# Performance work log

Hardware: AMD Instinct MI355X
Metric: run time of the kernel (lower is better)

Reference implementation:

```python
import jax, jax.numpy as jnp
import numpy as np

HIDDEN = 64
ALPHA = 0.2  # leaky relu negative slope
NEG_INF = -9e15


def setup_inputs() -> dict:
    key = jax.random.key(0)
    k1, k2, k3, k4, k5 = jax.random.split(key, 5)
    b, N, Fin, Fout = 8, 2048, 512, 256
    inp = jax.random.normal(k1, (b, N, Fin), dtype=jnp.float32)
    adj = jax.random.randint(k2, (b, N, N), 0, 2, dtype=jnp.int32)
    # xavier_uniform with gain=1.414 ~ uniform(-lim, lim)
    def xavier(k, shape):
        lim = 1.414 * np.sqrt(6.0 / (shape[0] + shape[1]))
        return jax.random.uniform(k, shape, jnp.float32, -lim, lim)
    weight = xavier(k3, (Fin, Fout))
    ht = xavier(k4, (Fout, HIDDEN))
    a = xavier(k5, (2 * HIDDEN, 1))
    return {"input": inp, "adj": adj, "weight": weight, "ht": ht, "a": a}


def reference(input, adj, weight, ht, a):
    # h: [b, N, Fout]
    h = jnp.matmul(input, weight)
    # trans_h: [b, N, HIDDEN]
    trans_h = jnp.einsum('bnc,ck->bnk', h, ht)
    # The original cat([th_i, th_j]) @ a decomposes as th_i@a1 + th_j@a2
    a1, a2 = a[:HIDDEN, 0], a[HIDDEN:, 0]
    f1 = trans_h @ a1  # [b, N] source (row) term
    f2 = trans_h @ a2  # [b, N] target (col) term
    e = f1[:, :, None] + f2[:, None, :]  # [b, N, N]
    e = jnp.where(e >= 0, e, ALPHA * e)  # leaky relu
    scores = jnp.where(adj > 0, e, NEG_INF)
    attention = jax.nn.softmax(scores, axis=2)
    # dropout is identity in eval mode (deterministic reference)
    h_prime = jnp.matmul(attention, h)  # [b, N, Fout]
    return jax.nn.elu(h_prime)  # concat=True
```

## Files before the change

kernel.cpp:

```cpp
#include <hip/hip_runtime.h>

typedef float f32x4 __attribute__((ext_vector_type(4)));
typedef short s16x8 __attribute__((ext_vector_type(8)));
typedef unsigned short u16x4 __attribute__((ext_vector_type(4)));

#define NB 8
#define NN 2048
#define FIN 512
#define FOUT 256

__device__ __forceinline__ unsigned short f2bf(float f) {
  unsigned u = __builtin_bit_cast(unsigned, f);
  u += 0x7fffu + ((u >> 16) & 1u);
  return (unsigned short)(u >> 16);
}

__global__ void prep_vecs_k(const float* __restrict__ W, const float* __restrict__ HT,
                            const float* __restrict__ A, float* __restrict__ v1,
                            float* __restrict__ v2) {
  __shared__ float w1[256], w2[256];
  int t = threadIdx.x;
  float s1 = 0.f, s2 = 0.f;
  for (int k = 0; k < 64; k++) {
    float h = HT[t * 64 + k];
    s1 += h * A[k];
    s2 += h * A[64 + k];
  }
  w1[t] = s1;
  w2[t] = s2;
  __syncthreads();
  for (int c = t; c < FIN; c += 256) {
    float a1 = 0.f, a2 = 0.f;
    for (int f = 0; f < FOUT; f++) {
      float w = W[c * FOUT + f];
      a1 += w * w1[f];
      a2 += w * w2[f];
    }
    v1[c] = a1;
    v2[c] = a2;
  }
}

__global__ void prep_wT_k(const float* __restrict__ W, unsigned short* __restrict__ wT) {
  int id = blockIdx.x * 256 + threadIdx.x;
  int f = id >> 9, c = id & 511;
  wT[id] = f2bf(W[c * FOUT + f]);
}

__global__ void f12_k(const float* __restrict__ inp, const float* __restrict__ v1,
                      const float* __restrict__ v2, float* __restrict__ f1,
                      float* __restrict__ f2) {
  int row = blockIdx.x * 4 + (threadIdx.x >> 6);
  int lane = threadIdx.x & 63;
  const float* rp = inp + (size_t)row * FIN + lane * 8;
  float4 x0 = *(const float4*)rp;
  float4 x1 = *(const float4*)(rp + 4);
  float4 a0 = *(const float4*)(v1 + lane * 8);
  float4 a1 = *(const float4*)(v1 + lane * 8 + 4);
  float4 b0 = *(const float4*)(v2 + lane * 8);
  float4 b1 = *(const float4*)(v2 + lane * 8 + 4);
  float s1 = x0.x * a0.x + x0.y * a0.y + x0.z * a0.z + x0.w * a0.w +
             x1.x * a1.x + x1.y * a1.y + x1.z * a1.z + x1.w * a1.w;
  float s2 = x0.x * b0.x + x0.y * b0.y + x0.z * b0.z + x0.w * b0.w +
             x1.x * b1.x + x1.y * b1.y + x1.z * b1.z + x1.w * b1.w;
  for (int o = 32; o > 0; o >>= 1) {
    s1 += __shfl_xor(s1, o);
    s2 += __shfl_xor(s2, o);
  }
  if (lane == 0) {
    f1[row] = s1;
    f2[row] = s2;
  }
}

__global__ __launch_bounds__(512) void gemm1_k(const float* __restrict__ inp,
                                               const unsigned short* __restrict__ wT,
                                               unsigned short* __restrict__ hT) {
  int tid = threadIdx.x;
  int w = tid >> 6, l = tid & 63, lr = l & 15, lg = l >> 4;
  int jtile = blockIdx.x * 64;
  f32x4 acc[2][4] = {};
  for (int c0 = 0; c0 < FIN; c0 += 32) {
    s16x8 af[2];
#pragma unroll
    for (int mf = 0; mf < 2; mf++) {
      int f = w * 32 + mf * 16 + lr;
      af[mf] = *(const s16x8*)(wT + (size_t)f * FIN + c0 + lg * 8);
    }
    s16x8 bfv[4];
#pragma unroll
    for (int nf = 0; nf < 4; nf++) {
      int jg = jtile + nf * 16 + lr;
      const float* p = inp + (size_t)jg * FIN + c0 + lg * 8;
      float4 x0 = *(const float4*)p;
      float4 x1 = *(const float4*)(p + 4);
      s16x8 t;
      t[0] = (short)f2bf(x0.x); t[1] = (short)f2bf(x0.y);
      t[2] = (short)f2bf(x0.z); t[3] = (short)f2bf(x0.w);
      t[4] = (short)f2bf(x1.x); t[5] = (short)f2bf(x1.y);
      t[6] = (short)f2bf(x1.z); t[7] = (short)f2bf(x1.w);
      bfv[nf] = t;
    }
#pragma unroll
    for (int mf = 0; mf < 2; mf++)
#pragma unroll
      for (int nf = 0; nf < 4; nf++)
        acc[mf][nf] =
            __builtin_amdgcn_mfma_f32_16x16x32_bf16(af[mf], bfv[nf], acc[mf][nf], 0, 0, 0);
  }
  int bb = jtile >> 11, jl = jtile & 2047;
#pragma unroll
  for (int mf = 0; mf < 2; mf++)
#pragma unroll
    for (int nf = 0; nf < 4; nf++)
#pragma unroll
      for (int r = 0; r < 4; r++) {
        int f = w * 32 + mf * 16 + lg * 4 + r;
        int j = jl + nf * 16 + lr;
        hT[((size_t)bb * FOUT + f) * (size_t)NN + j] = f2bf(acc[mf][nf][r]);
      }
}

__global__ __launch_bounds__(512) void pv_k(const int* __restrict__ adj,
                                            const unsigned short* __restrict__ hT,
                                            const float* __restrict__ f1,
                                            const float* __restrict__ f2,
                                            float* __restrict__ out) {
  __shared__ float f2s[NN];
  __shared__ float f1s[64];
  __shared__ float lsum[64];
  __shared__ unsigned short ptile[64 * 32];

  int tid = threadIdx.x;
  int b = blockIdx.x >> 5;
  int itile = (blockIdx.x & 31) * 64;

  for (int k = tid; k < NN; k += 512) f2s[k] = f2[b * NN + k];
  if (tid < 64) f1s[tid] = f1[b * NN + itile + tid];
  __syncthreads();

  int w = tid >> 6, l = tid & 63, lr = l & 15, lg = l >> 4;
  int wm = w >> 2, wn = w & 3;
  int iloc = tid >> 3, s8 = tid & 7;

  const int* adjrow = adj + ((size_t)(b * NN + itile + iloc)) * NN + s8 * 4;
  const unsigned short* hTb = hT + (size_t)b * FOUT * NN;
  float fi = f1s[iloc];
  float ls = 0.f;
  f32x4 acc[2][4] = {};

  char* pbase = (char*)ptile;
  int wr_off = iloc * 64 + ((((s8 >> 1) ^ (iloc & 3)) << 4) | ((s8 & 1) << 3));

  int4 adv = *(const int4*)adjrow;
  for (int jb = 0; jb < NN; jb += 32) {
    float4 fv = *(const float4*)&f2s[jb + s8 * 4];
    u16x4 pb;
    {
      float e0 = fi + fv.x, e1 = fi + fv.y, e2 = fi + fv.z, e3 = fi + fv.w;
      e0 = fmaxf(e0, 0.2f * e0);
      e1 = fmaxf(e1, 0.2f * e1);
      e2 = fmaxf(e2, 0.2f * e2);
      e3 = fmaxf(e3, 0.2f * e3);
      float p0 = (adv.x > 0) ? __expf(e0) : 0.f;
      float p1 = (adv.y > 0) ? __expf(e1) : 0.f;
      float p2 = (adv.z > 0) ? __expf(e2) : 0.f;
      float p3 = (adv.w > 0) ? __expf(e3) : 0.f;
      ls += p0 + p1 + p2 + p3;
      pb[0] = f2bf(p0); pb[1] = f2bf(p1); pb[2] = f2bf(p2); pb[3] = f2bf(p3);
    }
    *(u16x4*)(pbase + wr_off) = pb;

    if (jb + 32 < NN) adv = *(const int4*)(adjrow + jb + 32);

    s16x8 bfr[4];
#pragma unroll
    for (int nf = 0; nf < 4; nf++) {
      int f = wn * 64 + nf * 16 + lr;
      bfr[nf] = *(const s16x8*)(hTb + (size_t)f * NN + jb + lg * 8);
    }

    __syncthreads();

    s16x8 afr[2];
#pragma unroll
    for (int mf = 0; mf < 2; mf++) {
      int i = wm * 32 + mf * 16 + lr;
      afr[mf] = *(s16x8*)(pbase + i * 64 + ((lg ^ (i & 3)) << 4));
    }
#pragma unroll
    for (int mf = 0; mf < 2; mf++)
#pragma unroll
      for (int nf = 0; nf < 4; nf++)
        acc[mf][nf] =
            __builtin_amdgcn_mfma_f32_16x16x32_bf16(afr[mf], bfr[nf], acc[mf][nf], 0, 0, 0);

    __syncthreads();
  }

  ls += __shfl_xor(ls, 1);
  ls += __shfl_xor(ls, 2);
  ls += __shfl_xor(ls, 4);
  if (s8 == 0) lsum[iloc] = ls;
  __syncthreads();

#pragma unroll
  for (int mf = 0; mf < 2; mf++)
#pragma unroll
    for (int nf = 0; nf < 4; nf++)
#pragma unroll
      for (int r = 0; r < 4; r++) {
        int i = wm * 32 + mf * 16 + lg * 4 + r;
        int fcol = wn * 64 + nf * 16 + lr;
        float v = acc[mf][nf][r] / lsum[i];
        v = (v > 0.f) ? v : expm1f(v);
        out[((size_t)(b * NN + itile + i)) * FOUT + fcol] = v;
      }
}

extern "C" void kernel_launch(void* const* d_in, const int* in_sizes, int n_in,
                              void* d_out, int out_size, void* d_ws, size_t ws_size,
                              hipStream_t stream) {
  const float* inp = (const float*)d_in[0];
  const int* adj   = (const int*)d_in[1];
  const float* W   = (const float*)d_in[2];
  const float* HT  = (const float*)d_in[3];
  const float* A   = (const float*)d_in[4];
  float* out = (float*)d_out;

  char* ws = (char*)d_ws;
  float* v1 = (float*)ws;
  float* v2 = v1 + 512;
  float* f1 = (float*)(ws + 4096);
  float* f2 = (float*)(ws + 69632);
  unsigned short* wT = (unsigned short*)(ws + 135168);
  unsigned short* hT = (unsigned short*)(ws + 397312);

  hipLaunchKernelGGL(prep_vecs_k, dim3(1), dim3(256), 0, stream, W, HT, A, v1, v2);
  hipLaunchKernelGGL(prep_wT_k, dim3(512), dim3(256), 0, stream, W, wT);
  hipLaunchKernelGGL(f12_k, dim3(4096), dim3(256), 0, stream, inp, v1, v2, f1, f2);
  hipLaunchKernelGGL(gemm1_k, dim3(256), dim3(512), 0, stream, inp, wT, hT);
  hipLaunchKernelGGL(pv_k, dim3(256), dim3(512), 0, stream, adj, hT, f1, f2, out);
}
```

Measured before the change: 143.8 us.

## Fuse f1/f2 into gemm1 and restructure attention kernel to register-only P fragments

```diff
diff --git a/kernel.cpp b/kernel.cpp
--- a/kernel.cpp
+++ b/kernel.cpp
@@ -2,17 +2,29 @@
 
 typedef float f32x4 __attribute__((ext_vector_type(4)));
 typedef short s16x8 __attribute__((ext_vector_type(8)));
-typedef unsigned short u16x4 __attribute__((ext_vector_type(4)));
 
 #define NB 8
 #define NN 2048
 #define FIN 512
 #define FOUT 256
+#define L2E 1.4426950408889634f
+
+#if __has_builtin(__builtin_amdgcn_exp2f)
+#define EXP2(x) __builtin_amdgcn_exp2f(x)
+#else
+#define EXP2(x) __expf((x)*0.6931471805599453f)
+#endif
 
 __device__ __forceinline__ unsigned short f2bf(float f) {
   unsigned u = __builtin_bit_cast(unsigned, f);
   u += 0x7fffu + ((u >> 16) & 1u);
   return (unsigned short)(u >> 16);
+}
+
+__device__ __forceinline__ unsigned pkbf(float lo, float hi) {
+  unsigned r;
+  asm("v_cvt_pk_bf16_f32 %0, %1, %2" : "=v"(r) : "v"(lo), "v"(hi));
+  return r;
 }
 
 __global__ void prep_vecs_k(const float* __restrict__ W, const float* __restrict__ HT,
@@ -47,45 +59,31 @@
   wT[id] = f2bf(W[c * FOUT + f]);
 }
 
-__global__ void f12_k(const float* __restrict__ inp, const float* __restrict__ v1,
-                      const float* __restrict__ v2, float* __restrict__ f1,
-                      float* __restrict__ f2) {
-  int row = blockIdx.x * 4 + (threadIdx.x >> 6);
-  int lane = threadIdx.x & 63;
-  const float* rp = inp + (size_t)row * FIN + lane * 8;
-  float4 x0 = *(const float4*)rp;
-  float4 x1 = *(const float4*)(rp + 4);
-  float4 a0 = *(const float4*)(v1 + lane * 8);
-  float4 a1 = *(const float4*)(v1 + lane * 8 + 4);
-  float4 b0 = *(const float4*)(v2 + lane * 8);
-  float4 b1 = *(const float4*)(v2 + lane * 8 + 4);
-  float s1 = x0.x * a0.x + x0.y * a0.y + x0.z * a0.z + x0.w * a0.w +
-             x1.x * a1.x + x1.y * a1.y + x1.z * a1.z + x1.w * a1.w;
-  float s2 = x0.x * b0.x + x0.y * b0.y + x0.z * b0.z + x0.w * b0.w +
-             x1.x * b1.x + x1.y * b1.y + x1.z * b1.z + x1.w * b1.w;
-  for (int o = 32; o > 0; o >>= 1) {
-    s1 += __shfl_xor(s1, o);
-    s2 += __shfl_xor(s2, o);
-  }
-  if (lane == 0) {
-    f1[row] = s1;
-    f2[row] = s2;
-  }
-}
-
 __global__ __launch_bounds__(512) void gemm1_k(const float* __restrict__ inp,
                                                const unsigned short* __restrict__ wT,
-                                               unsigned short* __restrict__ hT) {
+                                               unsigned short* __restrict__ hT,
+                                               const float* __restrict__ v1,
+                                               const float* __restrict__ v2,
+                                               float* __restrict__ f1,
+                                               float* __restrict__ f2) {
   int tid = threadIdx.x;
   int w = tid >> 6, l = tid & 63, lr = l & 15, lg = l >> 4;
   int jtile = blockIdx.x * 64;
   f32x4 acc[2][4] = {};
+  float s1[4] = {0.f, 0.f, 0.f, 0.f}, s2[4] = {0.f, 0.f, 0.f, 0.f};
   for (int c0 = 0; c0 < FIN; c0 += 32) {
     s16x8 af[2];
 #pragma unroll
     for (int mf = 0; mf < 2; mf++) {
       int f = w * 32 + mf * 16 + lr;
       af[mf] = *(const s16x8*)(wT + (size_t)f * FIN + c0 + lg * 8);
+    }
+    float4 va0, va1, vb0, vb1;
+    if (w == 0) {
+      va0 = *(const float4*)(v1 + c0 + lg * 8);
+      va1 = *(const float4*)(v1 + c0 + lg * 8 + 4);
+      vb0 = *(const float4*)(v2 + c0 + lg * 8);
+      vb1 = *(const float4*)(v2 + c0 + lg * 8 + 4);
     }
     s16x8 bfv[4];
 #pragma unroll
@@ -100,6 +98,12 @@
       t[4] = (short)f2bf(x1.x); t[5] = (short)f2bf(x1.y);
       t[6] = (short)f2bf(x1.z); t[7] = (short)f2bf(x1.w);
       bfv[nf] = t;
+      if (w == 0) {
+        s1[nf] += x0.x * va0.x + x0.y * va0.y + x0.z * va0.z + x0.w * va0.w +
+                  x1.x * va1.x + x1.y * va1.y + x1.z * va1.z + x1.w * va1.w;
+        s2[nf] += x0.x * vb0.x + x0.y * vb0.y + x0.z * vb0.z + x0.w * vb0.w +
+                  x1.x * vb1.x + x1.y * vb1.y + x1.z * vb1.z + x1.w * vb1.w;
+      }
     }
 #pragma unroll
     for (int mf = 0; mf < 2; mf++)
@@ -119,103 +123,131 @@
         int j = jl + nf * 16 + lr;
         hT[((size_t)bb * FOUT + f) * (size_t)NN + j] = f2bf(acc[mf][nf][r]);
       }
-}
-
-__global__ __launch_bounds__(512) void pv_k(const int* __restrict__ adj,
-                                            const unsigned short* __restrict__ hT,
-                                            const float* __restrict__ f1,
-                                            const float* __restrict__ f2,
-                                            float* __restrict__ out) {
-  __shared__ float f2s[NN];
-  __shared__ float f1s[64];
-  __shared__ float lsum[64];
-  __shared__ unsigned short ptile[64 * 32];
-
+  if (w == 0) {
+#pragma unroll
+    for (int nf = 0; nf < 4; nf++) {
+      float a = s1[nf], b = s2[nf];
+      a += __shfl_xor(a, 16); a += __shfl_xor(a, 32);
+      b += __shfl_xor(b, 16); b += __shfl_xor(b, 32);
+      if (lg == 0) {
+        int jg = jtile + nf * 16 + lr;
+        f1[jg] = a * L2E;
+        f2[jg] = b * L2E;
+      }
+    }
+  }
+}
+
+__global__ __launch_bounds__(256, 2) void pv_k(const int* __restrict__ adj,
+                                               const unsigned short* __restrict__ hT,
+                                               const float* __restrict__ f1,
+                                               const float* __restrict__ f2,
+                                               float* __restrict__ out) {
   int tid = threadIdx.x;
-  int b = blockIdx.x >> 5;
-  int itile = (blockIdx.x & 31) * 64;
-
-  for (int k = tid; k < NN; k += 512) f2s[k] = f2[b * NN + k];
-  if (tid < 64) f1s[tid] = f1[b * NN + itile + tid];
-  __syncthreads();
-
-  int w = tid >> 6, l = tid & 63, lr = l & 15, lg = l >> 4;
-  int wm = w >> 2, wn = w & 3;
-  int iloc = tid >> 3, s8 = tid & 7;
-
-  const int* adjrow = adj + ((size_t)(b * NN + itile + iloc)) * NN + s8 * 4;
+  int w = tid >> 6;
+  int l = tid & 63, lr = l & 15, lg = l >> 4;
+  int blk = blockIdx.x;
+  int b = blk >> 6;
+  int i0 = (blk & 63) * 32;
+  int f0 = w * 64;
+  int ja = lg * 8;
+
+  const int* arow0 = adj + ((size_t)(b * NN + i0 + lr)) * NN + ja;
+  const int* arow1 = arow0 + (size_t)16 * NN;
   const unsigned short* hTb = hT + (size_t)b * FOUT * NN;
-  float fi = f1s[iloc];
-  float ls = 0.f;
+  const float* f2b = f2 + b * NN + ja;
+  float fi0 = f1[b * NN + i0 + lr];
+  float fi1 = f1[b * NN + i0 + 16 + lr];
+
   f32x4 acc[2][4] = {};
-
-  char* pbase = (char*)ptile;
-  int wr_off = iloc * 64 + ((((s8 >> 1) ^ (iloc & 3)) << 4) | ((s8 & 1) << 3));
-
-  int4 adv = *(const int4*)adjrow;
-  for (int jb = 0; jb < NN; jb += 32) {
-    float4 fv = *(const float4*)&f2s[jb + s8 * 4];
-    u16x4 pb;
-    {
-      float e0 = fi + fv.x, e1 = fi + fv.y, e2 = fi + fv.z, e3 = fi + fv.w;
-      e0 = fmaxf(e0, 0.2f * e0);
-      e1 = fmaxf(e1, 0.2f * e1);
-      e2 = fmaxf(e2, 0.2f * e2);
-      e3 = fmaxf(e3, 0.2f * e3);
-      float p0 = (adv.x > 0) ? __expf(e0) : 0.f;
-      float p1 = (adv.y > 0) ? __expf(e1) : 0.f;
-      float p2 = (adv.z > 0) ? __expf(e2) : 0.f;
-      float p3 = (adv.w > 0) ? __expf(e3) : 0.f;
-      ls += p0 + p1 + p2 + p3;
-      pb[0] = f2bf(p0); pb[1] = f2bf(p1); pb[2] = f2bf(p2); pb[3] = f2bf(p3);
-    }
-    *(u16x4*)(pbase + wr_off) = pb;
-
-    if (jb + 32 < NN) adv = *(const int4*)(adjrow + jb + 32);
-
-    s16x8 bfr[4];
-#pragma unroll
-    for (int nf = 0; nf < 4; nf++) {
-      int f = wn * 64 + nf * 16 + lr;
-      bfr[nf] = *(const s16x8*)(hTb + (size_t)f * NN + jb + lg * 8);
-    }
-
-    __syncthreads();
-
-    s16x8 afr[2];
-#pragma unroll
-    for (int mf = 0; mf < 2; mf++) {
-      int i = wm * 32 + mf * 16 + lr;
-      afr[mf] = *(s16x8*)(pbase + i * 64 + ((lg ^ (i & 3)) << 4));
-    }
-#pragma unroll
-    for (int mf = 0; mf < 2; mf++)
-#pragma unroll
-      for (int nf = 0; nf < 4; nf++)
-        acc[mf][nf] =
-            __builtin_amdgcn_mfma_f32_16x16x32_bf16(afr[mf], bfr[nf], acc[mf][nf], 0, 0, 0);
-
-    __syncthreads();
-  }
-
-  ls += __shfl_xor(ls, 1);
-  ls += __shfl_xor(ls, 2);
-  ls += __shfl_xor(ls, 4);
-  if (s8 == 0) lsum[iloc] = ls;
-  __syncthreads();
-
-#pragma unroll
-  for (int mf = 0; mf < 2; mf++)
-#pragma unroll
-    for (int nf = 0; nf < 4; nf++)
-#pragma unroll
-      for (int r = 0; r < 4; r++) {
-        int i = wm * 32 + mf * 16 + lg * 4 + r;
-        int fcol = wn * 64 + nf * 16 + lr;
-        float v = acc[mf][nf][r] / lsum[i];
-        v = (v > 0.f) ? v : expm1f(v);
-        out[((size_t)(b * NN + itile + i)) * FOUT + fcol] = v;
-      }
+  float ls0 = 0.f, ls1 = 0.f;
+
+  auto pcomp = [&](float fi, const int4& mA, const int4& mB, const float4& fA,
+                   const float4& fB, float& ls) -> s16x8 {
+    float e0 = fi + fA.x, e1 = fi + fA.y, e2 = fi + fA.z, e3 = fi + fA.w;
+    float e4 = fi + fB.x, e5 = fi + fB.y, e6 = fi + fB.z, e7 = fi + fB.w;
+    e0 = fmaxf(e0, 0.2f * e0); e1 = fmaxf(e1, 0.2f * e1);
+    e2 = fmaxf(e2, 0.2f * e2); e3 = fmaxf(e3, 0.2f * e3);
+    e4 = fmaxf(e4, 0.2f * e4); e5 = fmaxf(e5, 0.2f * e5);
+    e6 = fmaxf(e6, 0.2f * e6); e7 = fmaxf(e7, 0.2f * e7);
+    float p0 = (mA.x > 0) ? EXP2(e0) : 0.f;
+    float p1 = (mA.y > 0) ? EXP2(e1) : 0.f;
+    float p2 = (mA.z > 0) ? EXP2(e2) : 0.f;
+    float p3 = (mA.w > 0) ? EXP2(e3) : 0.f;
+    float p4 = (mB.x > 0) ? EXP2(e4) : 0.f;
+    float p5 = (mB.y > 0) ? EXP2(e5) : 0.f;
+    float p6 = (mB.z > 0) ? EXP2(e6) : 0.f;
+    float p7 = (mB.w > 0) ? EXP2(e7) : 0.f;
+    ls += ((p0 + p1) + (p2 + p3)) + ((p4 + p5) + (p6 + p7));
+    union { unsigned u[4]; s16x8 v; } pk;
+    pk.u[0] = pkbf(p0, p1); pk.u[1] = pkbf(p2, p3);
+    pk.u[2] = pkbf(p4, p5); pk.u[3] = pkbf(p6, p7);
+    return pk.v;
+  };
+
+  auto body = [&](int jb, int4& r0A, int4& r0B, int4& r1A, int4& r1B, float4& pfA,
+                  float4& pfB) {
+    const unsigned short* hp = hTb + (size_t)(f0 + lr) * NN + jb + ja;
+    s16x8 b0 = *(const s16x8*)(hp);
+    s16x8 b1 = *(const s16x8*)(hp + 16 * NN);
+    s16x8 b2 = *(const s16x8*)(hp + 32 * NN);
+    s16x8 b3 = *(const s16x8*)(hp + 48 * NN);
+    int4 c0A = r0A, c0B = r0B, c1A = r1A, c1B = r1B;
+    float4 fA = pfA, fB = pfB;
+    if (jb + 64 < NN) {
+      r0A = *(const int4*)(arow0 + jb + 64);
+      r0B = *(const int4*)(arow0 + jb + 68);
+      r1A = *(const int4*)(arow1 + jb + 64);
+      r1B = *(const int4*)(arow1 + jb + 68);
+      pfA = *(const float4*)(f2b + jb + 64);
+      pfB = *(const float4*)(f2b + jb + 68);
+    }
+    s16x8 af0 = pcomp(fi0, c0A, c0B, fA, fB, ls0);
+    s16x8 af1 = pcomp(fi1, c1A, c1B, fA, fB, ls1);
+    acc[0][0] = __builtin_amdgcn_mfma_f32_16x16x32_bf16(af0, b0, acc[0][0], 0, 0, 0);
+    acc[0][1] = __builtin_amdgcn_mfma_f32_16x16x32_bf16(af0, b1, acc[0][1], 0, 0, 0);
+    acc[0][2] = __builtin_amdgcn_mfma_f32_16x16x32_bf16(af0, b2, acc[0][2], 0, 0, 0);
+    acc[0][3] = __builtin_amdgcn_mfma_f32_16x16x32_bf16(af0, b3, acc[0][3], 0, 0, 0);
+    acc[1][0] = __builtin_amdgcn_mfma_f32_16x16x32_bf16(af1, b0, acc[1][0], 0, 0, 0);
+    acc[1][1] = __builtin_amdgcn_mfma_f32_16x16x32_bf16(af1, b1, acc[1][1], 0, 0, 0);
+    acc[1][2] = __builtin_amdgcn_mfma_f32_16x16x32_bf16(af1, b2, acc[1][2], 0, 0, 0);
+    acc[1][3] = __builtin_amdgcn_mfma_f32_16x16x32_bf16(af1, b3, acc[1][3], 0, 0, 0);
+  };
+
+  int4 s0_0A = *(const int4*)(arow0 + 0), s0_0B = *(const int4*)(arow0 + 4);
+  int4 s0_1A = *(const int4*)(arow1 + 0), s0_1B = *(const int4*)(arow1 + 4);
+  float4 s0_fA = *(const float4*)(f2b + 0), s0_fB = *(const float4*)(f2b + 4);
+  int4 s1_0A = *(const int4*)(arow0 + 32), s1_0B = *(const int4*)(arow0 + 36);
+  int4 s1_1A = *(const int4*)(arow1 + 32), s1_1B = *(const int4*)(arow1 + 36);
+  float4 s1_fA = *(const float4*)(f2b + 32), s1_fB = *(const float4*)(f2b + 36);
+
+  for (int jb = 0; jb < NN; jb += 64) {
+    body(jb, s0_0A, s0_0B, s0_1A, s0_1B, s0_fA, s0_fB);
+    body(jb + 32, s1_0A, s1_0B, s1_1A, s1_1B, s1_fA, s1_fB);
+  }
+
+  ls0 += __shfl_xor(ls0, 16); ls0 += __shfl_xor(ls0, 32);
+  ls1 += __shfl_xor(ls1, 16); ls1 += __shfl_xor(ls1, 32);
+  float rd0[4], rd1[4];
+#pragma unroll
+  for (int r = 0; r < 4; r++) {
+    rd0[r] = 1.0f / __shfl(ls0, lg * 4 + r);
+    rd1[r] = 1.0f / __shfl(ls1, lg * 4 + r);
+  }
+
+#pragma unroll
+  for (int nf = 0; nf < 4; nf++)
+#pragma unroll
+    for (int r = 0; r < 4; r++) {
+      int m0 = lg * 4 + r;
+      int fcol = f0 + nf * 16 + lr;
+      float v0 = acc[0][nf][r] * rd0[r];
+      v0 = (v0 > 0.f) ? v0 : expm1f(v0);
+      out[((size_t)(b * NN + i0 + m0)) * FOUT + fcol] = v0;
+      float v1_ = acc[1][nf][r] * rd1[r];
+      v1_ = (v1_ > 0.f) ? v1_ : expm1f(v1_);
+      out[((size_t)(b * NN + i0 + 16 + m0)) * FOUT + fcol] = v1_;
+    }
 }
 
 extern "C" void kernel_launch(void* const* d_in, const int* in_sizes, int n_in,
@@ -238,7 +270,6 @@
 
   hipLaunchKernelGGL(prep_vecs_k, dim3(1), dim3(256), 0, stream, W, HT, A, v1, v2);
   hipLaunchKernelGGL(prep_wT_k, dim3(512), dim3(256), 0, stream, W, wT);
-  hipLaunchKernelGGL(f12_k, dim3(4096), dim3(256), 0, stream, inp, v1, v2, f1, f2);
-  hipLaunchKernelGGL(gemm1_k, dim3(256), dim3(512), 0, stream, inp, wT, hT);
-  hipLaunchKernelGGL(pv_k, dim3(256), dim3(512), 0, stream, adj, hT, f1, f2, out);
-}
+  hipLaunchKernelGGL(gemm1_k, dim3(256), dim3(512), 0, stream, inp, wT, hT, v1, v2, f1, f2);
+  hipLaunchKernelGGL(pv_k, dim3(512), dim3(256), 0, stream, adj, hT, f1, f2, out);
+}
```

Result: slower. 207.2 us (+44.0%).
